# Optimization experiments

Measured on AMD Instinct MI355X. Metric: run time of the kernel, lower is better.

The kernel has to match this reference:

```python
import jax, jax.numpy as jnp
import numpy as np

RHO, MU, DT = 1.0, 0.1, 4.0
AX_X, AX_Y = -1, -2  # x = last axis, y = second-to-last


def first_derivative(f, ax, scheme):
    # unit grid spacing; boundary wrap is irrelevant since [1:-1,1:-1] is sliced off
    if scheme == 'left':
        return f - jnp.roll(f, 1, ax)
    if scheme == 'right':
        return jnp.roll(f, -1, ax) - f
    return 0.5 * (jnp.roll(f, -1, ax) - jnp.roll(f, 1, ax))  # central


def vel_map(f, ax, side):
    # staggered-grid interpolation of velocity to neighboring face
    if side == 'left':
        return 0.5 * (f + jnp.roll(f, 1, ax))
    return 0.5 * (f + jnp.roll(f, -1, ax))


def laplacian(f):
    return (jnp.roll(f, 1, AX_X) + jnp.roll(f, -1, AX_X)
            + jnp.roll(f, 1, AX_Y) + jnp.roll(f, -1, AX_Y) - 4.0 * f)


def setup_inputs() -> dict:
    key = jax.random.key(0)
    k1, k2, k3, k4 = jax.random.split(key, 4)
    B, H, W = 8, 1024, 1024
    return {
        'v_old': jax.random.normal(k1, (B, 2, H, W), dtype=jnp.float32),
        'v_new': jax.random.normal(k2, (B, 2, H, W), dtype=jnp.float32),
        'p_new': jax.random.normal(k3, (B, 1, H, W), dtype=jnp.float32),
        'flow_mask_mac': jax.random.randint(k4, (B, 1, H, W), 0, 2).astype(jnp.int32),
    }


def reference(v_old, v_new, p_new, flow_mask_mac):
    mask = flow_mask_mac.astype(v_old.dtype)
    v = 0.5 * (v_new + v_old)  # integration == 'imex'

    u_old, w_old = v_old[:, 0:1], v_old[:, 1:2]
    u_new, w_new = v_new[:, 0:1], v_new[:, 1:2]
    u, w = v[:, 0:1], v[:, 1:2]

    # x-momentum residual (channel 1)
    res_x = mask * (RHO * ((w_new - w_old) / DT
                           + w * first_derivative(w, AX_X, 'central')
                           + 0.5 * (vel_map(u, AX_X, 'left') * first_derivative(w, AX_Y, 'left')
                                    + vel_map(u, AX_X, 'right') * first_derivative(w, AX_Y, 'right')))
                    + first_derivative(p_new, AX_X, 'left')
                    - MU * laplacian(w))

    # y-momentum residual (channel 0)
    res_y = mask * (RHO * ((u_new - u_old) / DT
                           + u * first_derivative(u, AX_Y, 'central')
                           + 0.5 * (vel_map(w, AX_Y, 'left') * first_derivative(u, AX_X, 'left')
                                    + vel_map(w, AX_Y, 'right') * first_derivative(u, AX_X, 'right')))
                    + first_derivative(p_new, AX_Y, 'left')
                    - MU * laplacian(u))

    loss_x = jnp.mean(jnp.square(res_x)[:, :, 1:-1, 1:-1], axis=(1, 2, 3))
    loss_y = jnp.mean(jnp.square(res_y)[:, :, 1:-1, 1:-1], axis=(1, 2, 3))
    return loss_x + loss_y  # shape [B]
```

## Files before the change

### kernel.cpp

```cpp
#include <hip/hip_runtime.h>


#define NS_H 1024
#define NS_W 1024
#define RY   8
#define NBY  128
#define PARTS_PER_B NBY

__device__ __forceinline__ float4 ld4(const float* p) { return *(const float4*)p; }
__device__ __forceinline__ int4  ld4i(const int* p)   { return *(const int4*)p; }
__device__ __forceinline__ float4 avg4(float4 a, float4 b) {
    return make_float4(0.5f*(a.x+b.x), 0.5f*(a.y+b.y), 0.5f*(a.z+b.z), 0.5f*(a.w+b.w));
}
__device__ __forceinline__ float4 sub4(float4 a, float4 b) {
    return make_float4(a.x-b.x, a.y-b.y, a.z-b.z, a.w-b.w);
}

__global__ __launch_bounds__(256, 3) void ns_loss_partial(
    const float* __restrict__ v_old,
    const float* __restrict__ v_new,
    const float* __restrict__ p,
    const int*   __restrict__ mask,
    float* __restrict__ ws)
{
    const int blk = blockIdx.x;
    const int b   = blk / NBY;
    const int cy  = blk % NBY;
    const int y0  = 1 + cy * RY;
    const int ny  = min(RY, (NS_H - 1) - y0);

    const size_t hw = (size_t)NS_H * NS_W;
    const float* uo = v_old + (size_t)b * 2 * hw;
    const float* wo = uo + hw;
    const float* un = v_new + (size_t)b * 2 * hw;
    const float* wn = un + hw;
    const float* pb = p    + (size_t)b * hw;
    const int*   mb = mask + (size_t)b * hw;

    const int tid  = (int)threadIdx.x;
    const int lane = tid & 63;
    const int x0   = tid * 4;
    const bool seamL = (lane == 0)  && (x0 > 0);
    const bool seamR = (lane == 63) && (x0 + 4 < NS_W);

    const int off_m = (y0 - 1) * NS_W + x0;
    const int off_c = off_m + NS_W;
    const int off_p = off_c + NS_W;
    const int off_q = off_p + NS_W;

    float4 t0 = ld4(un + off_m), t1 = ld4(uo + off_m);
    float4 t2 = ld4(wn + off_m), t3 = ld4(wo + off_m);
    float4 t4 = ld4(un + off_c), t5 = ld4(uo + off_c);
    float4 t6 = ld4(wn + off_c), t7 = ld4(wo + off_c);
    float4 t8 = ld4(un + off_p), t9 = ld4(uo + off_p);
    float4 ta = ld4(wn + off_p), tb = ld4(wo + off_p);
    float4 p_m4 = ld4(pb + off_m);
    float4 p_c4 = ld4(pb + off_c);
    int4   m_c4 = ld4i(mb + off_c);

    float4 u_m = avg4(t0, t1), w_m = avg4(t2, t3);
    float4 u_c = avg4(t4, t5), du_c = sub4(t4, t5);
    float4 w_c = avg4(t6, t7), dw_c = sub4(t6, t7);
    float4 u_p = avg4(t8, t9), du_p = sub4(t8, t9);
    float4 w_p = avg4(ta, tb), dw_p = sub4(ta, tb);

    float s_ul = 0.f, s_wl = 0.f, s_pl = 0.f, s_ur = 0.f, s_wr = 0.f;
    if (seamL) {
        s_ul = 0.5f * (un[off_c - 1] + uo[off_c - 1]);
        s_wl = 0.5f * (wn[off_c - 1] + wo[off_c - 1]);
        s_pl = pb[off_c - 1];
    }
    if (seamR) {
        s_ur = 0.5f * (un[off_c + 4] + uo[off_c + 4]);
        s_wr = 0.5f * (wn[off_c + 4] + wo[off_c + 4]);
    }

    float4 f_un = ld4(un + off_q), f_uo = ld4(uo + off_q);
    float4 f_wn = ld4(wn + off_q), f_wo = ld4(wo + off_q);
    float4 f_p  = ld4(pb + off_p);
    int4   f_m  = ld4i(mb + off_p);
    float f_ul = 0.f, f_wl = 0.f, f_pl = 0.f, f_ur = 0.f, f_wr = 0.f;
    if (seamL) {
        f_ul = 0.5f * (un[off_p - 1] + uo[off_p - 1]);
        f_wl = 0.5f * (wn[off_p - 1] + wo[off_p - 1]);
        f_pl = pb[off_p - 1];
    }
    if (seamR) {
        f_ur = 0.5f * (un[off_p + 4] + uo[off_p + 4]);
        f_wr = 0.5f * (wn[off_p + 4] + wo[off_p + 4]);
    }

    float acc = 0.f;

    for (int r = 0; r < ny; ++r) {
        float ul = __shfl_up(u_c.w, 1);   if (lane == 0)  ul = s_ul;
        float wl = __shfl_up(w_c.w, 1);   if (lane == 0)  wl = s_wl;
        float pl = __shfl_up(p_c4.w, 1);  if (lane == 0)  pl = s_pl;
        float ur = __shfl_down(u_c.x, 1); if (lane == 63) ur = s_ur;
        float wr = __shfl_down(w_c.x, 1); if (lane == 63) wr = s_wr;

        {
            const float uc[6]  = {ul, u_c.x, u_c.y, u_c.z, u_c.w, ur};
            const float wcv[6] = {wl, w_c.x, w_c.y, w_c.z, w_c.w, wr};
            const float uym[4] = {u_m.x, u_m.y, u_m.z, u_m.w};
            const float uyp[4] = {u_p.x, u_p.y, u_p.z, u_p.w};
            const float wym[4] = {w_m.x, w_m.y, w_m.z, w_m.w};
            const float wyp[4] = {w_p.x, w_p.y, w_p.z, w_p.w};
            const float du[4]  = {du_c.x, du_c.y, du_c.z, du_c.w};
            const float dw[4]  = {dw_c.x, dw_c.y, dw_c.z, dw_c.w};
            const float pcv[5] = {pl, p_c4.x, p_c4.y, p_c4.z, p_c4.w};
            const float pym[4] = {p_m4.x, p_m4.y, p_m4.z, p_m4.w};
            const int   mm[4]  = {m_c4.x, m_c4.y, m_c4.z, m_c4.w};

            #pragma unroll
            for (int j = 0; j < 4; ++j) {
                const int x = x0 + j;
                const float m = (x >= 1 && x <= NS_W - 2) ? (float)mm[j] : 0.f;
                const float u_cc = uc[j+1],  u_xm = uc[j],  u_xp = uc[j+2];
                const float w_cc = wcv[j+1], w_xm = wcv[j], w_xp = wcv[j+2];

                float res_x =
                    dw[j] * 0.25f
                  + w_cc * 0.5f * (w_xp - w_xm)
                  + 0.5f * ( 0.5f * (u_cc + u_xm) * (w_cc   - wym[j])
                           + 0.5f * (u_cc + u_xp) * (wyp[j] - w_cc  ) )
                  + (pcv[j+1] - pcv[j])
                  - 0.1f * (w_xm + w_xp + wym[j] + wyp[j] - 4.f * w_cc);

                float res_y =
                    du[j] * 0.25f
                  + u_cc * 0.5f * (uyp[j] - uym[j])
                  + 0.5f * ( 0.5f * (w_cc + wym[j]) * (u_cc - u_xm)
                           + 0.5f * (w_cc + wyp[j]) * (u_xp - u_cc) )
                  + (pcv[j+1] - pym[j])
                  - 0.1f * (u_xm + u_xp + uym[j] + uyp[j] - 4.f * u_cc);

                acc += m * (res_x * res_x + res_y * res_y);
            }
        }

        u_m = u_c;  w_m = w_c;
        u_c = u_p;  w_c = w_p;  du_c = du_p;  dw_c = dw_p;
        u_p = avg4(f_un, f_uo); du_p = sub4(f_un, f_uo);
        w_p = avg4(f_wn, f_wo); dw_p = sub4(f_wn, f_wo);
        p_m4 = p_c4; p_c4 = f_p; m_c4 = f_m;
        s_ul = f_ul; s_wl = f_wl; s_pl = f_pl; s_ur = f_ur; s_wr = f_wr;

        int row_q = y0 + r + 3; if (row_q > NS_H - 1) row_q = NS_H - 1;
        int row_n = y0 + r + 2; if (row_n > NS_H - 1) row_n = NS_H - 1;
        const int off_q2 = row_q * NS_W + x0;
        const int off_n  = row_n * NS_W + x0;
        f_un = ld4(un + off_q2); f_uo = ld4(uo + off_q2);
        f_wn = ld4(wn + off_q2); f_wo = ld4(wo + off_q2);
        f_p  = ld4(pb + off_n);
        f_m  = ld4i(mb + off_n);
        if (seamL) {
            f_ul = 0.5f * (un[off_n - 1] + uo[off_n - 1]);
            f_wl = 0.5f * (wn[off_n - 1] + wo[off_n - 1]);
            f_pl = pb[off_n - 1];
        }
        if (seamR) {
            f_ur = 0.5f * (un[off_n + 4] + uo[off_n + 4]);
            f_wr = 0.5f * (wn[off_n + 4] + wo[off_n + 4]);
        }
    }

    #pragma unroll
    for (int off = 32; off > 0; off >>= 1)
        acc += __shfl_down(acc, off);

    __shared__ float smem[4];
    const int wid = tid >> 6;
    if (lane == 0) smem[wid] = acc;
    __syncthreads();

    if (tid == 0)
        ws[blk] = smem[0] + smem[1] + smem[2] + smem[3];
}

__global__ __launch_bounds__(256) void ns_loss_reduce(
    const float* __restrict__ ws, float* __restrict__ out)
{
    const int b = blockIdx.x;
    float acc = 0.f;
    for (int i = threadIdx.x; i < PARTS_PER_B; i += 256)
        acc += ws[b * PARTS_PER_B + i];

    #pragma unroll
    for (int off = 32; off > 0; off >>= 1)
        acc += __shfl_down(acc, off);

    __shared__ float smem[4];
    const int lane = threadIdx.x & 63;
    const int wid  = threadIdx.x >> 6;
    if (lane == 0) smem[wid] = acc;
    __syncthreads();

    if (threadIdx.x == 0) {
        const float inv = 1.0f / ((float)(NS_H - 2) * (float)(NS_W - 2));
        out[b] = (smem[0] + smem[1] + smem[2] + smem[3]) * inv;
    }
}

extern "C" void kernel_launch(void* const* d_in, const int* in_sizes, int n_in,
                              void* d_out, int out_size, void* d_ws, size_t ws_size,
                              hipStream_t stream) {
    const float* v_old = (const float*)d_in[0];
    const float* v_new = (const float*)d_in[1];
    const float* p_new = (const float*)d_in[2];
    const int*   msk   = (const int*)d_in[3];
    float* out = (float*)d_out;
    float* ws  = (float*)d_ws;

    const int B = out_size;

    ns_loss_partial<<<dim3(B * NBY), dim3(256), 0, stream>>>(v_old, v_new, p_new, msk, ws);
    ns_loss_reduce<<<dim3(B), dim3(256), 0, stream>>>(ws, out);
}
```

Measured before the change: 207.5 us.

## Exchange wave seam values through LDS and prefetch rows two ahead

The uncoalesced scalar global loads at the left and right wave seams are replaced by an LDS exchange between neighbouring wavefronts. This exchange uses a double-buffered edge array and a __syncthreads per row. The row loop is unrolled by two with two register prefetch buffers, so global loads run two rows ahead of the compute. The aim is more memory-level parallelism and fewer scattered loads, at the cost of one block barrier per row and more registers.

```diff
diff --git a/kernel.cpp b/kernel.cpp
--- a/kernel.cpp
+++ b/kernel.cpp
@@ -39,14 +39,14 @@
 
     const int tid  = (int)threadIdx.x;
     const int lane = tid & 63;
+    const int wid  = tid >> 6;
     const int x0   = tid * 4;
-    const bool seamL = (lane == 0)  && (x0 > 0);
-    const bool seamR = (lane == 63) && (x0 + 4 < NS_W);
+
+    __shared__ float edge[2][4][8];
 
     const int off_m = (y0 - 1) * NS_W + x0;
     const int off_c = off_m + NS_W;
     const int off_p = off_c + NS_W;
-    const int off_q = off_p + NS_W;
 
     float4 t0 = ld4(un + off_m), t1 = ld4(uo + off_m);
     float4 t2 = ld4(wn + off_m), t3 = ld4(wo + off_m);
@@ -58,46 +58,44 @@
     float4 p_c4 = ld4(pb + off_c);
     int4   m_c4 = ld4i(mb + off_c);
 
+    const int offAv = (y0 + 2) * NS_W + x0, offAn = (y0 + 1) * NS_W + x0;
+    const int offBv = (y0 + 3) * NS_W + x0, offBn = (y0 + 2) * NS_W + x0;
+    float4 a_un = ld4(un + offAv), a_uo = ld4(uo + offAv);
+    float4 a_wn = ld4(wn + offAv), a_wo = ld4(wo + offAv);
+    float4 a_p  = ld4(pb + offAn); int4 a_m = ld4i(mb + offAn);
+    float4 b_un = ld4(un + offBv), b_uo = ld4(uo + offBv);
+    float4 b_wn = ld4(wn + offBv), b_wo = ld4(wo + offBv);
+    float4 b_p  = ld4(pb + offBn); int4 b_m = ld4i(mb + offBn);
+
     float4 u_m = avg4(t0, t1), w_m = avg4(t2, t3);
     float4 u_c = avg4(t4, t5), du_c = sub4(t4, t5);
     float4 w_c = avg4(t6, t7), dw_c = sub4(t6, t7);
     float4 u_p = avg4(t8, t9), du_p = sub4(t8, t9);
     float4 w_p = avg4(ta, tb), dw_p = sub4(ta, tb);
 
-    float s_ul = 0.f, s_wl = 0.f, s_pl = 0.f, s_ur = 0.f, s_wr = 0.f;
-    if (seamL) {
-        s_ul = 0.5f * (un[off_c - 1] + uo[off_c - 1]);
-        s_wl = 0.5f * (wn[off_c - 1] + wo[off_c - 1]);
-        s_pl = pb[off_c - 1];
-    }
-    if (seamR) {
-        s_ur = 0.5f * (un[off_c + 4] + uo[off_c + 4]);
-        s_wr = 0.5f * (wn[off_c + 4] + wo[off_c + 4]);
-    }
-
-    float4 f_un = ld4(un + off_q), f_uo = ld4(uo + off_q);
-    float4 f_wn = ld4(wn + off_q), f_wo = ld4(wo + off_q);
-    float4 f_p  = ld4(pb + off_p);
-    int4   f_m  = ld4i(mb + off_p);
-    float f_ul = 0.f, f_wl = 0.f, f_pl = 0.f, f_ur = 0.f, f_wr = 0.f;
-    if (seamL) {
-        f_ul = 0.5f * (un[off_p - 1] + uo[off_p - 1]);
-        f_wl = 0.5f * (wn[off_p - 1] + wo[off_p - 1]);
-        f_pl = pb[off_p - 1];
-    }
-    if (seamR) {
-        f_ur = 0.5f * (un[off_p + 4] + uo[off_p + 4]);
-        f_wr = 0.5f * (wn[off_p + 4] + wo[off_p + 4]);
-    }
-
     float acc = 0.f;
 
-    for (int r = 0; r < ny; ++r) {
-        float ul = __shfl_up(u_c.w, 1);   if (lane == 0)  ul = s_ul;
-        float wl = __shfl_up(w_c.w, 1);   if (lane == 0)  wl = s_wl;
-        float pl = __shfl_up(p_c4.w, 1);  if (lane == 0)  pl = s_pl;
-        float ur = __shfl_down(u_c.x, 1); if (lane == 63) ur = s_ur;
-        float wr = __shfl_down(w_c.x, 1); if (lane == 63) wr = s_wr;
+    auto iter = [&](int r, float4& g_un, float4& g_uo, float4& g_wn, float4& g_wo,
+                    float4& g_p, int4& g_m) {
+        const int y   = y0 + r;
+        const int par = r & 1;
+
+        if (lane == 63) {
+            edge[par][wid][0] = u_c.w; edge[par][wid][1] = w_c.w; edge[par][wid][2] = p_c4.w;
+        }
+        if (lane == 0) {
+            edge[par][wid][3] = u_c.x; edge[par][wid][4] = w_c.x;
+        }
+        __syncthreads();
+
+        float ul = __shfl_up(u_c.w, 1), wl = __shfl_up(w_c.w, 1), pl = __shfl_up(p_c4.w, 1);
+        if (lane == 0 && wid > 0) {
+            ul = edge[par][wid-1][0]; wl = edge[par][wid-1][1]; pl = edge[par][wid-1][2];
+        }
+        float ur = __shfl_down(u_c.x, 1), wr = __shfl_down(w_c.x, 1);
+        if (lane == 63 && wid < 3) {
+            ur = edge[par][wid+1][3]; wr = edge[par][wid+1][4];
+        }
 
         {
             const float uc[6]  = {ul, u_c.x, u_c.y, u_c.z, u_c.w, ur};
@@ -141,28 +139,22 @@
 
         u_m = u_c;  w_m = w_c;
         u_c = u_p;  w_c = w_p;  du_c = du_p;  dw_c = dw_p;
-        u_p = avg4(f_un, f_uo); du_p = sub4(f_un, f_uo);
-        w_p = avg4(f_wn, f_wo); dw_p = sub4(f_wn, f_wo);
-        p_m4 = p_c4; p_c4 = f_p; m_c4 = f_m;
-        s_ul = f_ul; s_wl = f_wl; s_pl = f_pl; s_ur = f_ur; s_wr = f_wr;
-
-        int row_q = y0 + r + 3; if (row_q > NS_H - 1) row_q = NS_H - 1;
-        int row_n = y0 + r + 2; if (row_n > NS_H - 1) row_n = NS_H - 1;
-        const int off_q2 = row_q * NS_W + x0;
-        const int off_n  = row_n * NS_W + x0;
-        f_un = ld4(un + off_q2); f_uo = ld4(uo + off_q2);
-        f_wn = ld4(wn + off_q2); f_wo = ld4(wo + off_q2);
-        f_p  = ld4(pb + off_n);
-        f_m  = ld4i(mb + off_n);
-        if (seamL) {
-            f_ul = 0.5f * (un[off_n - 1] + uo[off_n - 1]);
-            f_wl = 0.5f * (wn[off_n - 1] + wo[off_n - 1]);
-            f_pl = pb[off_n - 1];
-        }
-        if (seamR) {
-            f_ur = 0.5f * (un[off_n + 4] + uo[off_n + 4]);
-            f_wr = 0.5f * (wn[off_n + 4] + wo[off_n + 4]);
-        }
+        u_p = avg4(g_un, g_uo); du_p = sub4(g_un, g_uo);
+        w_p = avg4(g_wn, g_wo); dw_p = sub4(g_wn, g_wo);
+        p_m4 = p_c4; p_c4 = g_p; m_c4 = g_m;
+
+        int rv = y + 4; if (rv > NS_H - 1) rv = NS_H - 1;
+        int rn = y + 3; if (rn > NS_H - 1) rn = NS_H - 1;
+        const int ov = rv * NS_W + x0;
+        const int on = rn * NS_W + x0;
+        g_un = ld4(un + ov); g_uo = ld4(uo + ov);
+        g_wn = ld4(wn + ov); g_wo = ld4(wo + ov);
+        g_p  = ld4(pb + on); g_m  = ld4i(mb + on);
+    };
+
+    for (int r = 0; r + 1 < ny; r += 2) {
+        iter(r,     a_un, a_uo, a_wn, a_wo, a_p, a_m);
+        iter(r + 1, b_un, b_uo, b_wn, b_wo, b_p, b_m);
     }
 
     #pragma unroll
@@ -170,7 +162,6 @@
         acc += __shfl_down(acc, off);
 
     __shared__ float smem[4];
-    const int wid = tid >> 6;
     if (lane == 0) smem[wid] = acc;
     __syncthreads();
 
```

Result: faster. 198.6 us (-4.3%).
